# Performance work log

Hardware: AMD Instinct MI355X
Metric: run time of the kernel (lower is better)

The kernel has to match this reference:

```python
import jax, jax.numpy as jnp
import numpy as np
import math

PHI = (1.0 + math.sqrt(5.0)) / 2.0
LN_EPS = 1e-5


def _carrier_phases(n_heads: int) -> np.ndarray:
    """Reproduce DimensionalHeadManager._allocate carrier phases."""
    base = [k * math.pi / 7.0 for k in range(7)]  # rung base phases
    n_rungs = 7
    raw = []
    remaining = n_heads
    for i in range(n_rungs):
        if i < n_rungs - 1:
            c = max(1, round(n_heads / PHI ** (i + 1)))
            c = min(c, remaining - (n_rungs - 1 - i))
            raw.append(c)
            remaining -= c
        else:
            raw.append(max(1, remaining))
    phases = []
    for rung_idx, count in enumerate(raw):
        for j in range(count):
            phases.append(base[rung_idx] + 2.0 * math.pi / max(count, 1) * j)
    return np.asarray(phases[:n_heads], dtype=np.float32)


def setup_inputs() -> dict:
    key = jax.random.key(0)
    ks = jax.random.split(key, 7)
    B, S, D, H = 2, 2048, 1024, 16
    w_scale = 0.02  # realistic init scale for Linear weights
    x = jax.random.normal(ks[0], (B, S, D), dtype=jnp.float32)
    Wq = jax.random.normal(ks[1], (D, D), dtype=jnp.float32) * w_scale
    Wk = jax.random.normal(ks[2], (D, D), dtype=jnp.float32) * w_scale
    Wv = jax.random.normal(ks[3], (D, D), dtype=jnp.float32) * w_scale
    Wo = jax.random.normal(ks[4], (D, D), dtype=jnp.float32) * w_scale
    Wp = jax.random.normal(ks[5], (D,), dtype=jnp.float32) * w_scale  # W_phase (1,D) flattened
    gamma = jnp.ones((D,), dtype=jnp.float32)
    beta = jnp.zeros((D,), dtype=jnp.float32)
    carrier = jnp.asarray(_carrier_phases(H))  # srl.carrier_freq init
    lam = jnp.float32(0.1)  # lambda_resonance init
    return {"x": x, "Wq": Wq, "Wk": Wk, "Wv": Wv, "Wo": Wo, "Wp": Wp,
            "gamma": gamma, "beta": beta, "carrier": carrier, "lam": lam}


def reference(x, Wq, Wk, Wv, Wo, Wp, gamma, beta, carrier, lam):
    B, S, D = x.shape
    H = carrier.shape[0]
    dh = D // H
    scale = 1.0 / math.sqrt(dh)

    residual = x
    # LayerNorm
    mu = jnp.mean(x, axis=-1, keepdims=True)
    var = jnp.mean((x - mu) ** 2, axis=-1, keepdims=True)
    xn = (x - mu) * jax.lax.rsqrt(var + LN_EPS) * gamma + beta

    # Q/K/V projections (torch Linear: y = x @ W.T), split into heads
    q = jnp.einsum('bsd,ed->bse', xn, Wq).reshape(B, S, H, dh)
    k = jnp.einsum('bsd,ed->bse', xn, Wk).reshape(B, S, H, dh)
    v = jnp.einsum('bsd,ed->bse', xn, Wv).reshape(B, S, H, dh)

    # scalar phase per token, per-head carrier resonance gate
    phase = jnp.einsum('bsd,d->bs', xn, Wp)                       # (B,S)
    head_T = jnp.cos((phase[..., None] - carrier) * 0.5) ** 2     # (B,S,H)

    # attention scores + resonance term R_ij = cos^2((phi_i - phi_j)/2)
    scores = jnp.einsum('bihd,bjhd->bhij', q, k) * scale          # (B,H,S,S)
    R = jnp.cos((phase[:, :, None] - phase[:, None, :]) * 0.5) ** 2  # (B,S,S)
    scores = scores + lam * R[:, None, :, :]

    attn = jax.nn.softmax(scores, axis=-1)
    out = jnp.einsum('bhij,bjhd->bihd', attn, v)                  # (B,S,H,dh)
    out = out * head_T[..., None]                                 # per-head resonance gating
    emergent_energy = jnp.sum(jnp.abs(out))
    y = residual + jnp.einsum('bse,de->bsd', out.reshape(B, S, D), Wo)
    return (y, emergent_energy)
```

## Files before the change

### kernel.cpp

```cpp
#include <hip/hip_runtime.h>
#include <hip/hip_bf16.h>

#define S_LEN 2048
#define D_MODEL 1024
#define NH 16
#define DH 64
#define M_TOK 4096
#define DK 80

typedef __attribute__((ext_vector_type(8))) short bf16x8;
typedef __attribute__((ext_vector_type(4))) float f32x4;
typedef __attribute__((ext_vector_type(16))) float f32x16;

#define LOG2E 1.4426950408889634f

__device__ __forceinline__ unsigned short f2bf(float f) {
  unsigned u = __float_as_uint(f);
  u += 0x7FFF + ((u >> 16) & 1);
  return (unsigned short)(u >> 16);
}

__device__ __forceinline__ void gl16(const void* g, void* l) {
  __builtin_amdgcn_global_load_lds(
      (const __attribute__((address_space(1))) unsigned int*)g,
      (__attribute__((address_space(3))) unsigned int*)l, 16, 0, 0);
}

__global__ __launch_bounds__(256) void prep_kernel(
    const float* __restrict__ Wq, const float* __restrict__ Wk,
    const float* __restrict__ Wv, const float* __restrict__ Wo,
    unsigned short* __restrict__ wbf, float* __restrict__ energy) {
  if (blockIdx.x == 0 && threadIdx.x == 0) *energy = 0.f;
  int idx = (blockIdx.x * 256 + threadIdx.x) * 4;
  int wsel = idx >> 20;
  const float* s = (wsel == 0) ? Wq : (wsel == 1) ? Wk : (wsel == 2) ? Wv : Wo;
  int off = idx & 1048575;
  float4 v = *(const float4*)(s + off);
  ushort4 p;
  p.x = f2bf(v.x); p.y = f2bf(v.y); p.z = f2bf(v.z); p.w = f2bf(v.w);
  *(ushort4*)(wbf + idx) = p;
}

__device__ __forceinline__ float block_sum(float v, float* sm) {
#pragma unroll
  for (int o = 32; o > 0; o >>= 1) v += __shfl_xor(v, o, 64);
  int w = threadIdx.x >> 6;
  __syncthreads();
  if ((threadIdx.x & 63) == 0) sm[w] = v;
  __syncthreads();
  return sm[0] + sm[1] + sm[2] + sm[3];
}

__global__ __launch_bounds__(256) void ln_phase_kernel(
    const float* __restrict__ x, const float* __restrict__ Wp,
    const float* __restrict__ gamma, const float* __restrict__ beta,
    unsigned short* __restrict__ xn, float* __restrict__ cosP,
    float* __restrict__ sinP, unsigned short* __restrict__ kk80) {
  __shared__ float sm[4];
  int row = blockIdx.x;
  int tid = threadIdx.x;
  float4 v = ((const float4*)(x + (size_t)row * D_MODEL))[tid];
  float mu = block_sum(v.x + v.y + v.z + v.w, sm) * (1.0f / D_MODEL);
  float d0 = v.x - mu, d1 = v.y - mu, d2 = v.z - mu, d3 = v.w - mu;
  float var = block_sum(d0 * d0 + d1 * d1 + d2 * d2 + d3 * d3, sm) * (1.0f / D_MODEL);
  float rinv = rsqrtf(var + 1e-5f);
  float4 g = ((const float4*)gamma)[tid];
  float4 be = ((const float4*)beta)[tid];
  float n0 = d0 * rinv * g.x + be.x;
  float n1 = d1 * rinv * g.y + be.y;
  float n2 = d2 * rinv * g.z + be.z;
  float n3 = d3 * rinv * g.w + be.w;
  ushort4 p;
  p.x = f2bf(n0); p.y = f2bf(n1); p.z = f2bf(n2); p.w = f2bf(n3);
  ((ushort4*)(xn + (size_t)row * D_MODEL))[tid] = p;
  float4 wp = ((const float4*)Wp)[tid];
  float ph = block_sum(n0 * wp.x + n1 * wp.y + n2 * wp.z + n3 * wp.w, sm);
  if (tid < 16) {
    float cp = cosf(ph), sp = sinf(ph);
    if (tid == 0) {
      cosP[row] = cp;
      sinP[row] = sp;
    }
    int b = row >> 11, s = row & (S_LEN - 1);
    unsigned int w0 = (unsigned int)f2bf(cp) | ((unsigned int)f2bf(sp) << 16);
    size_t gid = (size_t)(b * NH + tid) * S_LEN + s;
    *(int4*)(kk80 + gid * DK + 64) = make_int4((int)w0, 0, 0, 0);
  }
}

__global__ __launch_bounds__(256, 3) void qkv_gemm_kernel(
    const unsigned short* __restrict__ xn, const unsigned short* __restrict__ wbf,
    unsigned short* __restrict__ q, unsigned short* __restrict__ kk80,
    unsigned short* __restrict__ vT) {
  __shared__ __align__(16) unsigned short Sm[128 * 136];
  unsigned short* As = Sm;
  unsigned short* Bs = Sm + 128 * 64;
  int bid = blockIdx.x;
  bool vmode = bid >= 512;
  const unsigned short* Ap;
  const unsigned short* Bp;
  int m0, n0;
  if (!vmode) {
    m0 = (bid >> 4) * 128;
    n0 = (bid & 15) * 128;
    Ap = xn; Bp = wbf;
  } else {
    int v2 = bid - 512;
    m0 = (v2 & 7) * 128;
    n0 = (v2 >> 3) * 128;
    Ap = wbf + 2 * D_MODEL * D_MODEL; Bp = xn;
  }
  int tid = threadIdx.x;
  int wave = tid >> 6, lane = tid & 63, quad = lane >> 4, l15 = lane & 15;
  int wm = (wave & 1) * 64, wn = (wave >> 1) * 64;
  f32x4 acc[4][4];
#pragma unroll
  for (int r = 0; r < 4; ++r)
#pragma unroll
    for (int c = 0; c < 4; ++c) acc[r][c] = (f32x4){0.f, 0.f, 0.f, 0.f};

  for (int k0 = 0; k0 < D_MODEL; k0 += 64) {
    __syncthreads();
#pragma unroll
    for (int t = 0; t < 4; ++t) {
      int c = t * 256 + tid;
      int r = c >> 3, p = c & 7;
      int g = p ^ (r & 7);
      gl16(&Ap[(size_t)(m0 + r) * D_MODEL + k0 + g * 8], &As[c * 8]);
      gl16(&Bp[(size_t)(n0 + r) * D_MODEL + k0 + g * 8], &Bs[c * 8]);
    }
    __syncthreads();
    bf16x8 af[4][2], bfr[4][2];
#pragma unroll
    for (int r = 0; r < 4; ++r) {
      int R = wm + r * 16 + l15;
#pragma unroll
      for (int h = 0; h < 2; ++h)
        af[r][h] = *(const bf16x8*)&As[R * 64 + ((h * 4 + quad) ^ (R & 7)) * 8];
    }
#pragma unroll
    for (int c = 0; c < 4; ++c) {
      int R = wn + c * 16 + l15;
#pragma unroll
      for (int h = 0; h < 2; ++h)
        bfr[c][h] = *(const bf16x8*)&Bs[R * 64 + ((h * 4 + quad) ^ (R & 7)) * 8];
    }
#pragma unroll
    for (int h = 0; h < 2; ++h)
#pragma unroll
      for (int r = 0; r < 4; ++r)
#pragma unroll
        for (int c = 0; c < 4; ++c)
          acc[r][c] = __builtin_amdgcn_mfma_f32_16x16x32_bf16(af[r][h], bfr[c][h], acc[r][c], 0, 0, 0);
  }
  __syncthreads();
  float scl = (!vmode && n0 < 1024) ? (0.125f * LOG2E) : 1.0f;
#pragma unroll
  for (int r = 0; r < 4; ++r)
#pragma unroll
    for (int c = 0; c < 4; ++c)
#pragma unroll
      for (int rr = 0; rr < 4; ++rr) {
        int m = wm + r * 16 + quad * 4 + rr;
        int n = wn + c * 16 + l15;
        Sm[m * 136 + n] = f2bf(acc[r][c][rr] * scl);
      }
  __syncthreads();
  int r2 = tid >> 1, h64 = (tid & 1) * 64;
  const unsigned short* src = &Sm[r2 * 136 + h64];
  unsigned short* dst;
  if (!vmode) {
    int tok = m0 + r2;
    int bb = tok >> 11, ss = tok & (S_LEN - 1);
    int n = n0 + h64;
    if (n < 1024) {
      int hh = n >> 6;
      dst = q + (((size_t)(bb * NH + hh)) * S_LEN + ss) * DH;
    } else {
      int hh = (n >> 6) & 15;
      dst = kk80 + (((size_t)(bb * NH + hh)) * S_LEN + ss) * DK;
    }
  } else {
    int e = m0 + r2;
    int hh = e >> 6, d = e & 63;
    int tok = n0 + h64;
    int bb = tok >> 11, ss = tok & (S_LEN - 1);
    dst = vT + (((size_t)(bb * NH + hh)) * DH + d) * S_LEN + ss;
  }
#pragma unroll
  for (int i = 0; i < 8; ++i)
    *(int4*)(dst + i * 8) = *(const int4*)(src + i * 8);
}

__global__ __launch_bounds__(128, 3) void attn_kernel(
    const unsigned short* __restrict__ q, const unsigned short* __restrict__ kk80,
    const unsigned short* __restrict__ vT, const float* __restrict__ cosP,
    const float* __restrict__ sinP, const float* __restrict__ carrier,
    const float* __restrict__ lamp, unsigned short* __restrict__ outw,
    float* __restrict__ energy) {
  __shared__ __align__(16) unsigned short Ks[64 * 72];
  __shared__ __align__(16) unsigned short Vs[512 * 8];
  __shared__ __align__(16) unsigned int Ps[2][32 * 34];
  __shared__ float Lr[2][32];
  __shared__ float er[2];
  int bid = blockIdx.x;
  int xcd = bid & 7, g = bid >> 3;
  int bh = xcd * 4 + (g >> 5);
  int qt = g & 31;
  int b = bh >> 4, h = bh & 15;
  int tid = threadIdx.x, wave = tid >> 6, lane = tid & 63;
  int half = lane >> 5, l31 = lane & 31;

  const unsigned short* kb = kk80 + (size_t)bh * S_LEN * DK;
  const unsigned short* vb = vT + (size_t)bh * DH * S_LEN;
  int qrow = qt * 64 + wave * 32 + l31;

  bf16x8 bQ[5];
  {
    const unsigned short* qp = q + ((size_t)bh * S_LEN + qrow) * DH;
#pragma unroll
    for (int db = 0; db < 4; ++db)
      bQ[db] = *(const bf16x8*)(qp + db * 16 + half * 8);
    bf16x8 z8 = {0, 0, 0, 0, 0, 0, 0, 0};
    if (half == 0) {
      float hl2 = 0.5f * lamp[0] * LOG2E;
      z8[0] = (short)f2bf(hl2 * cosP[b * S_LEN + qrow]);
      z8[1] = (short)f2bf(hl2 * sinP[b * S_LEN + qrow]);
    }
    bQ[4] = z8;
  }

  f32x16 O0 = {}, O1 = {};
  float l_i = 0.f;

  for (int j0 = 0; j0 < S_LEN; j0 += 64) {
    __syncthreads();
#pragma unroll
    for (int t = 0; t < 4; ++t) {
      unsigned int cc = t * 128 + tid;
      unsigned int r = cc / 9u, p = cc - r * 9u;
      gl16(&kb[(size_t)(j0 + r) * DK + p * 8], (unsigned short*)Ks + cc * 8);
    }
    if (tid < 64) {
      unsigned int cc = 512 + tid;
      unsigned int r = cc / 9u, p = cc - r * 9u;
      gl16(&kb[(size_t)(j0 + r) * DK + p * 8], (unsigned short*)Ks + cc * 8);
    }
#pragma unroll
    for (int t = 0; t < 4; ++t) {
      int cc = t * 128 + tid;
      int r = cc >> 3, p = cc & 7;
      int g2 = p ^ (r & 7);
      gl16(&vb[(size_t)r * S_LEN + j0 + g2 * 8], (unsigned short*)Vs + cc * 8);
    }
    __syncthreads();

    f32x16 Sf[2];
#pragma unroll
    for (int sj = 0; sj < 2; ++sj) {
      Sf[sj] = (f32x16){};
      int r = sj * 32 + l31;
#pragma unroll
      for (int db = 0; db < 5; ++db) {
        int p = (db < 4) ? (db * 2 + half) : 8;
        bf16x8 aK = *(const bf16x8*)((const unsigned short*)Ks + (r * 9 + p) * 8);
        Sf[sj] = __builtin_amdgcn_mfma_f32_32x32x16_bf16(aK, bQ[db], Sf[sj], 0, 0, 0);
      }
    }

#pragma unroll
    for (int sj = 0; sj < 2; ++sj) {
#pragma unroll
      for (int rr = 0; rr < 8; ++rr) {
        float e0 = exp2f(Sf[sj][rr * 2 + 0]);
        float e1 = exp2f(Sf[sj][rr * 2 + 1]);
        l_i += e0 + e1;
        __hip_bfloat162 pk = __float22bfloat162_rn(float2{e0, e1});
        int jd = sj * 16 + (rr >> 1) * 4 + half * 2 + (rr & 1);
        Ps[wave][l31 * 34 + jd] = *(unsigned int*)&pk;
      }
    }

#pragma unroll
    for (int jb = 0; jb < 4; ++jb) {
      const unsigned int* pp = &Ps[wave][l31 * 34 + jb * 8 + half * 4];
      uint2 a0 = *(const uint2*)pp;
      uint2 a1 = *(const uint2*)(pp + 2);
      union { unsigned int u[4]; bf16x8 v; } cvt;
      cvt.u[0] = a0.x; cvt.u[1] = a0.y; cvt.u[2] = a1.x; cvt.u[3] = a1.y;
      {
        int rv = l31;
        int p = (jb * 2 + half) ^ (rv & 7);
        bf16x8 bV = *(const bf16x8*)((const unsigned short*)Vs + (rv * 8 + p) * 8);
        O0 = __builtin_amdgcn_mfma_f32_32x32x16_bf16(cvt.v, bV, O0, 0, 0, 0);
      }
      {
        int rv = 32 + l31;
        int p = (jb * 2 + half) ^ (rv & 7);
        bf16x8 bV = *(const bf16x8*)((const unsigned short*)Vs + (rv * 8 + p) * 8);
        O1 = __builtin_amdgcn_mfma_f32_32x32x16_bf16(cvt.v, bV, O1, 0, 0, 0);
      }
    }
  }

  l_i += __shfl_xor(l_i, 32, 64);
  Lr[wave][l31] = l_i;
  float ch = cosf(carrier[h]), sh = sinf(carrier[h]);
  float esum = 0.f;
#pragma unroll
  for (int reg = 0; reg < 16; ++reg) {
    int ir = (reg & 3) + 8 * (reg >> 2) + 4 * half;
    int srow = qt * 64 + wave * 32 + ir;
    float cp = cosP[b * S_LEN + srow], sp = sinP[b * S_LEN + srow];
    float gate = 0.5f + 0.5f * (cp * ch + sp * sh);
    float gl = gate / Lr[wave][ir];
    float v0 = O0[reg] * gl, v1 = O1[reg] * gl;
    esum += fabsf(v0) + fabsf(v1);
    size_t tok = (size_t)b * S_LEN + srow;
    outw[tok * D_MODEL + h * DH + l31] = f2bf(v0);
    outw[tok * D_MODEL + h * DH + 32 + l31] = f2bf(v1);
  }
#pragma unroll
  for (int off = 32; off > 0; off >>= 1) esum += __shfl_xor(esum, off, 64);
  if (lane == 0) er[wave] = esum;
  __syncthreads();
  if (tid == 0) atomicAdd(energy, er[0] + er[1]);
}

__global__ __launch_bounds__(256) void out_gemm_kernel(
    const unsigned short* __restrict__ A, const unsigned short* __restrict__ Wo,
    const float* __restrict__ x, float* __restrict__ y) {
  __shared__ __align__(16) unsigned short As[128 * 64];
  __shared__ __align__(16) unsigned short Bs[64 * 64];
  int tid = threadIdx.x;
  int wave = tid >> 6, lane = tid & 63, quad = lane >> 4, l15 = lane & 15;
  int wm = (wave & 1) * 64, wn = (wave >> 1) * 32;
  int m0 = blockIdx.y * 128, n0 = blockIdx.x * 64;
  f32x4 acc[4][2];
#pragma unroll
  for (int r = 0; r < 4; ++r)
#pragma unroll
    for (int c = 0; c < 2; ++c) acc[r][c] = (f32x4){0.f, 0.f, 0.f, 0.f};

  for (int k0 = 0; k0 < D_MODEL; k0 += 64) {
    __syncthreads();
#pragma unroll
    for (int t = 0; t < 4; ++t) {
      int c = t * 256 + tid;
      int r = c >> 3, p = c & 7;
      int qc = p ^ (r & 7);
      gl16(&A[(size_t)(m0 + r) * D_MODEL + k0 + qc * 8], &As[c * 8]);
    }
#pragma unroll
    for (int t = 0; t < 2; ++t) {
      int c = t * 256 + tid;
      int r = c >> 3, p = c & 7;
      int qc = p ^ (r & 7);
      gl16(&Wo[(size_t)(n0 + r) * D_MODEL + k0 + qc * 8], &Bs[c * 8]);
    }
    __syncthreads();
    bf16x8 af[4][2], bfr[2][2];
#pragma unroll
    for (int r = 0; r < 4; ++r) {
      int R = wm + r * 16 + l15;
#pragma unroll
      for (int h = 0; h < 2; ++h)
        af[r][h] = *(const bf16x8*)&As[R * 64 + ((h * 4 + quad) ^ (R & 7)) * 8];
    }
#pragma unroll
    for (int c = 0; c < 2; ++c) {
      int R = wn + c * 16 + l15;
#pragma unroll
      for (int h = 0; h < 2; ++h)
        bfr[c][h] = *(const bf16x8*)&Bs[R * 64 + ((h * 4 + quad) ^ (R & 7)) * 8];
    }
#pragma unroll
    for (int h = 0; h < 2; ++h)
#pragma unroll
      for (int r = 0; r < 4; ++r)
#pragma unroll
        for (int c = 0; c < 2; ++c)
          acc[r][c] = __builtin_amdgcn_mfma_f32_16x16x32_bf16(af[r][h], bfr[c][h], acc[r][c], 0, 0, 0);
  }
#pragma unroll
  for (int r = 0; r < 4; ++r) {
#pragma unroll
    for (int c = 0; c < 2; ++c) {
      int dcol = n0 + wn + c * 16 + l15;
#pragma unroll
      for (int rr = 0; rr < 4; ++rr) {
        int tok = m0 + wm + r * 16 + quad * 4 + rr;
        size_t idx = (size_t)tok * D_MODEL + dcol;
        y[idx] = x[idx] + acc[r][c][rr];
      }
    }
  }
}

extern "C" void kernel_launch(void* const* d_in, const int* in_sizes, int n_in,
                              void* d_out, int out_size, void* d_ws, size_t ws_size,
                              hipStream_t stream) {
  const float* x = (const float*)d_in[0];
  const float* Wq = (const float*)d_in[1];
  const float* Wk = (const float*)d_in[2];
  const float* Wv = (const float*)d_in[3];
  const float* Wo = (const float*)d_in[4];
  const float* Wp = (const float*)d_in[5];
  const float* gamma = (const float*)d_in[6];
  const float* beta = (const float*)d_in[7];
  const float* carrier = (const float*)d_in[8];
  const float* lam = (const float*)d_in[9];

  char* ws = (char*)d_ws;
  const size_t MB = 1024 * 1024;
  unsigned short* wbf = (unsigned short*)(ws);
  unsigned short* xn = (unsigned short*)(ws + 8 * MB);
  unsigned short* qq = (unsigned short*)(ws + 16 * MB);
  unsigned short* kk80 = (unsigned short*)(ws + 24 * MB);
  unsigned short* vT = (unsigned short*)(ws + 34 * MB);
  float* cosP = (float*)(ws + 42 * MB);
  float* sinP = (float*)(ws + 42 * MB + 16 * 1024);
  unsigned short* outw = xn;

  float* y = (float*)d_out;
  float* energy = y + (out_size - 1);

  prep_kernel<<<4096, 256, 0, stream>>>(Wq, Wk, Wv, Wo, wbf, energy);
  ln_phase_kernel<<<M_TOK, 256, 0, stream>>>(x, Wp, gamma, beta, xn, cosP, sinP,
                                             kk80);
  qkv_gemm_kernel<<<768, 256, 0, stream>>>(xn, wbf, qq, kk80, vT);
  attn_kernel<<<1024, 128, 0, stream>>>(qq, kk80, vT, cosP, sinP, carrier, lam,
                                        outw, energy);
  out_gemm_kernel<<<dim3(16, 32), 256, 0, stream>>>(outw, wbf + 3 * D_MODEL * D_MODEL,
                                                    x, y);
}
```

Measured before the change: 232.8 us.

## Double-buffer K/V tiles in attention and pass P via lane shuffles

The attention loop now keeps two LDS buffers for the K and V tiles. It issues the global-to-LDS loads for the next 64-key tile before computing on the current one, so load latency overlaps with MFMA and exp work, and one of the two barriers per iteration goes away. The P matrix is no longer staged through an LDS scratch buffer; it is repacked in registers with cross-lane xor shuffles to form the MFMA A operand. LDS use grows and the occupancy hint drops from 3 to 2 blocks per CU, which gives more registers but less latency hiding from concurrent blocks.

Result: slower. 241.2 us (+3.6%).

```diff
diff --git a/kernel.cpp b/kernel.cpp
--- a/kernel.cpp
+++ b/kernel.cpp
@@ -192,15 +192,14 @@
     *(int4*)(dst + i * 8) = *(const int4*)(src + i * 8);
 }
 
-__global__ __launch_bounds__(128, 3) void attn_kernel(
+__global__ __launch_bounds__(128, 2) void attn_kernel(
     const unsigned short* __restrict__ q, const unsigned short* __restrict__ kk80,
     const unsigned short* __restrict__ vT, const float* __restrict__ cosP,
     const float* __restrict__ sinP, const float* __restrict__ carrier,
     const float* __restrict__ lamp, unsigned short* __restrict__ outw,
     float* __restrict__ energy) {
-  __shared__ __align__(16) unsigned short Ks[64 * 72];
-  __shared__ __align__(16) unsigned short Vs[512 * 8];
-  __shared__ __align__(16) unsigned int Ps[2][32 * 34];
+  __shared__ __align__(16) unsigned short Ks[2][64 * 72];
+  __shared__ __align__(16) unsigned short Vs[2][512 * 8];
   __shared__ float Lr[2][32];
   __shared__ float er[2];
   int bid = blockIdx.x;
@@ -233,27 +232,37 @@
   f32x16 O0 = {}, O1 = {};
   float l_i = 0.f;
 
-  for (int j0 = 0; j0 < S_LEN; j0 += 64) {
+#define STAGE(buf, j0)                                                        \
+  {                                                                           \
+    unsigned short* Ksg = &Ks[buf][0];                                        \
+    unsigned short* Vsg = &Vs[buf][0];                                        \
+    _Pragma("unroll") for (int t = 0; t < 4; ++t) {                           \
+      unsigned int cc = t * 128 + tid;                                        \
+      unsigned int r = cc / 9u, p = cc - r * 9u;                              \
+      gl16(&kb[(size_t)((j0) + r) * DK + p * 8], Ksg + cc * 8);               \
+    }                                                                         \
+    if (tid < 64) {                                                           \
+      unsigned int cc = 512 + tid;                                            \
+      unsigned int r = cc / 9u, p = cc - r * 9u;                              \
+      gl16(&kb[(size_t)((j0) + r) * DK + p * 8], Ksg + cc * 8);               \
+    }                                                                         \
+    _Pragma("unroll") for (int t = 0; t < 4; ++t) {                           \
+      int cc = t * 128 + tid;                                                 \
+      int r = cc >> 3, p = cc & 7;                                            \
+      int g2 = p ^ (r & 7);                                                   \
+      gl16(&vb[(size_t)r * S_LEN + (j0) + g2 * 8], Vsg + cc * 8);             \
+    }                                                                         \
+  }
+
+  STAGE(0, 0);
+
+  for (int jt = 0; jt < 32; ++jt) {
+    int cur = jt & 1;
     __syncthreads();
-#pragma unroll
-    for (int t = 0; t < 4; ++t) {
-      unsigned int cc = t * 128 + tid;
-      unsigned int r = cc / 9u, p = cc - r * 9u;
-      gl16(&kb[(size_t)(j0 + r) * DK + p * 8], (unsigned short*)Ks + cc * 8);
-    }
-    if (tid < 64) {
-      unsigned int cc = 512 + tid;
-      unsigned int r = cc / 9u, p = cc - r * 9u;
-      gl16(&kb[(size_t)(j0 + r) * DK + p * 8], (unsigned short*)Ks + cc * 8);
-    }
-#pragma unroll
-    for (int t = 0; t < 4; ++t) {
-      int cc = t * 128 + tid;
-      int r = cc >> 3, p = cc & 7;
-      int g2 = p ^ (r & 7);
-      gl16(&vb[(size_t)r * S_LEN + j0 + g2 * 8], (unsigned short*)Vs + cc * 8);
-    }
-    __syncthreads();
+    if (jt + 1 < 32) STAGE(1 - cur, (jt + 1) * 64);
+
+    const unsigned short* Ksg = &Ks[cur][0];
+    const unsigned short* Vsg = &Vs[cur][0];
 
     f32x16 Sf[2];
 #pragma unroll
@@ -263,11 +272,12 @@
 #pragma unroll
       for (int db = 0; db < 5; ++db) {
         int p = (db < 4) ? (db * 2 + half) : 8;
-        bf16x8 aK = *(const bf16x8*)((const unsigned short*)Ks + (r * 9 + p) * 8);
+        bf16x8 aK = *(const bf16x8*)(Ksg + (r * 9 + p) * 8);
         Sf[sj] = __builtin_amdgcn_mfma_f32_32x32x16_bf16(aK, bQ[db], Sf[sj], 0, 0, 0);
       }
     }
 
+    unsigned int pk[2][8];
 #pragma unroll
     for (int sj = 0; sj < 2; ++sj) {
 #pragma unroll
@@ -275,29 +285,33 @@
         float e0 = exp2f(Sf[sj][rr * 2 + 0]);
         float e1 = exp2f(Sf[sj][rr * 2 + 1]);
         l_i += e0 + e1;
-        __hip_bfloat162 pk = __float22bfloat162_rn(float2{e0, e1});
-        int jd = sj * 16 + (rr >> 1) * 4 + half * 2 + (rr & 1);
-        Ps[wave][l31 * 34 + jd] = *(unsigned int*)&pk;
+        __hip_bfloat162 pc = __float22bfloat162_rn(float2{e0, e1});
+        pk[sj][rr] = *(unsigned int*)&pc;
       }
     }
 
 #pragma unroll
     for (int jb = 0; jb < 4; ++jb) {
-      const unsigned int* pp = &Ps[wave][l31 * 34 + jb * 8 + half * 4];
-      uint2 a0 = *(const uint2*)pp;
-      uint2 a1 = *(const uint2*)(pp + 2);
+      int sj = jb >> 1, base = (jb & 1) * 4;
+      unsigned int s0 = pk[sj][base + 0], s1 = pk[sj][base + 1];
+      unsigned int s2 = pk[sj][base + 2], s3 = pk[sj][base + 3];
+      unsigned int t0 = __shfl_xor(half ? s0 : s2, 32, 64);
+      unsigned int t1 = __shfl_xor(half ? s1 : s3, 32, 64);
       union { unsigned int u[4]; bf16x8 v; } cvt;
-      cvt.u[0] = a0.x; cvt.u[1] = a0.y; cvt.u[2] = a1.x; cvt.u[3] = a1.y;
+      cvt.u[0] = half ? t0 : s0;
+      cvt.u[1] = half ? t1 : s1;
+      cvt.u[2] = half ? s2 : t0;
+      cvt.u[3] = half ? s3 : t1;
       {
         int rv = l31;
         int p = (jb * 2 + half) ^ (rv & 7);
-        bf16x8 bV = *(const bf16x8*)((const unsigned short*)Vs + (rv * 8 + p) * 8);
+        bf16x8 bV = *(const bf16x8*)(Vsg + (rv * 8 + p) * 8);
         O0 = __builtin_amdgcn_mfma_f32_32x32x16_bf16(cvt.v, bV, O0, 0, 0, 0);
       }
       {
         int rv = 32 + l31;
         int p = (jb * 2 + half) ^ (rv & 7);
-        bf16x8 bV = *(const bf16x8*)((const unsigned short*)Vs + (rv * 8 + p) * 8);
+        bf16x8 bV = *(const bf16x8*)(Vsg + (rv * 8 + p) * 8);
         O1 = __builtin_amdgcn_mfma_f32_32x32x16_bf16(cvt.v, bV, O1, 0, 0, 0);
       }
     }
@@ -307,6 +321,7 @@
   Lr[wave][l31] = l_i;
   float ch = cosf(carrier[h]), sh = sinf(carrier[h]);
   float esum = 0.f;
+  __syncthreads();
 #pragma unroll
   for (int reg = 0; reg < 16; ++reg) {
     int ir = (reg & 3) + 8 * (reg >> 2) + 4 * half;
@@ -326,6 +341,7 @@
   __syncthreads();
   if (tid == 0) atomicAdd(energy, er[0] + er[1]);
 }
+#undef STAGE
 
 __global__ __launch_bounds__(256) void out_gemm_kernel(
     const unsigned short* __restrict__ A, const unsigned short* __restrict__ Wo,
```

## Split attention over key halves with merge kernel; pass P via shuffles

Applied to the files above, without the earlier changes.

Splits the attention key range into two halves so the grid doubles from 1024 to 2048 blocks, with a new merge kernel that sums the two unnormalized partial outputs and row sums, then applies the gate, normalization and energy reduction. The exp'd score tile is also rearranged into the PV MFMA operand layout with cross-half lane shuffles instead of an LDS round trip, which removes shared memory and a bank access path. The aim is better occupancy and load balance on the attention kernel. The cost is extra global traffic for the partial outputs, an extra kernel launch, and partials rounded to bf16 before they are merged.

Result: slower. 271.7 us (+16.7%).

```diff
diff --git a/kernel.cpp b/kernel.cpp
--- a/kernel.cpp
+++ b/kernel.cpp
@@ -18,6 +18,10 @@
   unsigned u = __float_as_uint(f);
   u += 0x7FFF + ((u >> 16) & 1);
   return (unsigned short)(u >> 16);
+}
+
+__device__ __forceinline__ float bf2f(unsigned short s) {
+  return __uint_as_float((unsigned)s << 16);
 }
 
 __device__ __forceinline__ void gl16(const void* g, void* l) {
@@ -192,21 +196,18 @@
     *(int4*)(dst + i * 8) = *(const int4*)(src + i * 8);
 }
 
-__global__ __launch_bounds__(128, 3) void attn_kernel(
+__global__ __launch_bounds__(128) void attn_kernel(
     const unsigned short* __restrict__ q, const unsigned short* __restrict__ kk80,
     const unsigned short* __restrict__ vT, const float* __restrict__ cosP,
-    const float* __restrict__ sinP, const float* __restrict__ carrier,
-    const float* __restrict__ lamp, unsigned short* __restrict__ outw,
-    float* __restrict__ energy) {
+    const float* __restrict__ sinP, const float* __restrict__ lamp,
+    unsigned short* __restrict__ Op0, unsigned short* __restrict__ Op1,
+    float* __restrict__ lp0, float* __restrict__ lp1) {
   __shared__ __align__(16) unsigned short Ks[64 * 72];
   __shared__ __align__(16) unsigned short Vs[512 * 8];
-  __shared__ __align__(16) unsigned int Ps[2][32 * 34];
-  __shared__ float Lr[2][32];
-  __shared__ float er[2];
   int bid = blockIdx.x;
   int xcd = bid & 7, g = bid >> 3;
-  int bh = xcd * 4 + (g >> 5);
-  int qt = g & 31;
+  int bh = xcd * 4 + (g >> 6);
+  int qt = (g & 63) >> 1, jh = g & 1;
   int b = bh >> 4, h = bh & 15;
   int tid = threadIdx.x, wave = tid >> 6, lane = tid & 63;
   int half = lane >> 5, l31 = lane & 31;
@@ -233,7 +234,8 @@
   f32x16 O0 = {}, O1 = {};
   float l_i = 0.f;
 
-  for (int j0 = 0; j0 < S_LEN; j0 += 64) {
+  for (int jt = 0; jt < 16; ++jt) {
+    int j0 = jh * (S_LEN / 2) + jt * 64;
     __syncthreads();
 #pragma unroll
     for (int t = 0; t < 4; ++t) {
@@ -268,6 +270,7 @@
       }
     }
 
+    unsigned int pk[2][8];
 #pragma unroll
     for (int sj = 0; sj < 2; ++sj) {
 #pragma unroll
@@ -275,19 +278,23 @@
         float e0 = exp2f(Sf[sj][rr * 2 + 0]);
         float e1 = exp2f(Sf[sj][rr * 2 + 1]);
         l_i += e0 + e1;
-        __hip_bfloat162 pk = __float22bfloat162_rn(float2{e0, e1});
-        int jd = sj * 16 + (rr >> 1) * 4 + half * 2 + (rr & 1);
-        Ps[wave][l31 * 34 + jd] = *(unsigned int*)&pk;
+        __hip_bfloat162 pc = __float22bfloat162_rn(float2{e0, e1});
+        pk[sj][rr] = *(unsigned int*)&pc;
       }
     }
 
 #pragma unroll
     for (int jb = 0; jb < 4; ++jb) {
-      const unsigned int* pp = &Ps[wave][l31 * 34 + jb * 8 + half * 4];
-      uint2 a0 = *(const uint2*)pp;
-      uint2 a1 = *(const uint2*)(pp + 2);
+      int sj = jb >> 1, base = (jb & 1) * 4;
+      unsigned int s0 = pk[sj][base + 0], s1 = pk[sj][base + 1];
+      unsigned int s2 = pk[sj][base + 2], s3 = pk[sj][base + 3];
+      unsigned int t0 = __shfl_xor(half ? s0 : s2, 32, 64);
+      unsigned int t1 = __shfl_xor(half ? s1 : s3, 32, 64);
       union { unsigned int u[4]; bf16x8 v; } cvt;
-      cvt.u[0] = a0.x; cvt.u[1] = a0.y; cvt.u[2] = a1.x; cvt.u[3] = a1.y;
+      cvt.u[0] = half ? t0 : s0;
+      cvt.u[1] = half ? t1 : s1;
+      cvt.u[2] = half ? s2 : t0;
+      cvt.u[3] = half ? s3 : t1;
       {
         int rv = l31;
         int p = (jb * 2 + half) ^ (rv & 7);
@@ -304,27 +311,54 @@
   }
 
   l_i += __shfl_xor(l_i, 32, 64);
-  Lr[wave][l31] = l_i;
-  float ch = cosf(carrier[h]), sh = sinf(carrier[h]);
-  float esum = 0.f;
+  unsigned short* Op = jh ? Op1 : Op0;
+  float* lp = jh ? lp1 : lp0;
+  size_t rowbase = (size_t)bh * S_LEN + qt * 64 + wave * 32;
+  if (half == 0) lp[rowbase + l31] = l_i;
 #pragma unroll
   for (int reg = 0; reg < 16; ++reg) {
     int ir = (reg & 3) + 8 * (reg >> 2) + 4 * half;
-    int srow = qt * 64 + wave * 32 + ir;
-    float cp = cosP[b * S_LEN + srow], sp = sinP[b * S_LEN + srow];
-    float gate = 0.5f + 0.5f * (cp * ch + sp * sh);
-    float gl = gate / Lr[wave][ir];
-    float v0 = O0[reg] * gl, v1 = O1[reg] * gl;
-    esum += fabsf(v0) + fabsf(v1);
-    size_t tok = (size_t)b * S_LEN + srow;
-    outw[tok * D_MODEL + h * DH + l31] = f2bf(v0);
-    outw[tok * D_MODEL + h * DH + 32 + l31] = f2bf(v1);
-  }
+    Op[(rowbase + ir) * 64 + l31] = f2bf(O0[reg]);
+    Op[(rowbase + ir) * 64 + 32 + l31] = f2bf(O1[reg]);
+  }
+}
+
+__global__ __launch_bounds__(256) void merge_kernel(
+    const unsigned short* __restrict__ Op0, const unsigned short* __restrict__ Op1,
+    const float* __restrict__ lp0, const float* __restrict__ lp1,
+    const float* __restrict__ cosP, const float* __restrict__ sinP,
+    const float* __restrict__ carrier, unsigned short* __restrict__ outw,
+    float* __restrict__ energy) {
+  __shared__ float er[4];
+  int tid = threadIdx.x;
+  size_t f = ((size_t)blockIdx.x * 256 + tid) * 8;
+  int row = (int)(f >> 6);
+  int c0 = (int)(f & 63);
+  int bh = row >> 11, s = row & (S_LEN - 1);
+  int b = bh >> 4, h = bh & 15;
+  float l = lp0[row] + lp1[row];
+  float cp = cosP[b * S_LEN + s], sp = sinP[b * S_LEN + s];
+  float ch = cosf(carrier[h]), sh = sinf(carrier[h]);
+  float gl = (0.5f + 0.5f * (cp * ch + sp * sh)) / l;
+  int4 a0 = *(const int4*)(Op0 + f);
+  int4 a1 = *(const int4*)(Op1 + f);
+  const unsigned short* u0 = (const unsigned short*)&a0;
+  const unsigned short* u1 = (const unsigned short*)&a1;
+  float esum = 0.f;
+  unsigned short ob[8];
+#pragma unroll
+  for (int i = 0; i < 8; ++i) {
+    float t = (bf2f(u0[i]) + bf2f(u1[i])) * gl;
+    esum += fabsf(t);
+    ob[i] = f2bf(t);
+  }
+  size_t tok = (size_t)b * S_LEN + s;
+  *(int4*)(outw + tok * D_MODEL + h * DH + c0) = *(int4*)&ob[0];
 #pragma unroll
   for (int off = 32; off > 0; off >>= 1) esum += __shfl_xor(esum, off, 64);
-  if (lane == 0) er[wave] = esum;
+  if ((tid & 63) == 0) er[tid >> 6] = esum;
   __syncthreads();
-  if (tid == 0) atomicAdd(energy, er[0] + er[1]);
+  if (tid == 0) atomicAdd(energy, er[0] + er[1] + er[2] + er[3]);
 }
 
 __global__ __launch_bounds__(256) void out_gemm_kernel(
@@ -420,7 +454,11 @@
   unsigned short* vT = (unsigned short*)(ws + 34 * MB);
   float* cosP = (float*)(ws + 42 * MB);
   float* sinP = (float*)(ws + 42 * MB + 16 * 1024);
-  unsigned short* outw = xn;
+  float* lp0 = (float*)(ws + 42 * MB + 64 * 1024);
+  float* lp1 = (float*)(ws + 42 * MB + 320 * 1024);
+  unsigned short* Op0 = xn;
+  unsigned short* Op1 = (unsigned short*)(ws + 43 * MB);
+  unsigned short* outw = (unsigned short*)(ws + 51 * MB);
 
   float* y = (float*)d_out;
   float* energy = y + (out_size - 1);
@@ -429,8 +467,10 @@
   ln_phase_kernel<<<M_TOK, 256, 0, stream>>>(x, Wp, gamma, beta, xn, cosP, sinP,
                                              kk80);
   qkv_gemm_kernel<<<768, 256, 0, stream>>>(xn, wbf, qq, kk80, vT);
-  attn_kernel<<<1024, 128, 0, stream>>>(qq, kk80, vT, cosP, sinP, carrier, lam,
-                                        outw, energy);
+  attn_kernel<<<2048, 128, 0, stream>>>(qq, kk80, vT, cosP, sinP, lam,
+                                        Op0, Op1, lp0, lp1);
+  merge_kernel<<<2048, 256, 0, stream>>>(Op0, Op1, lp0, lp1, cosP, sinP,
+                                         carrier, outw, energy);
   out_gemm_kernel<<<dim3(16, 32), 256, 0, stream>>>(outw, wbf + 3 * D_MODEL * D_MODEL,
                                                     x, y);
 }
```
